# Kernel tuning notes

Measured on AMD Instinct MI355X. Metric: run time of the kernel, lower is better.

## Reference

```python
import jax, jax.numpy as jnp
import numpy as np

C_Z = 128
C_HIDDEN = 128
N_RES = 384
B = 1
EPS = 1e-5


def _layernorm(x, w, b):
    mu = jnp.mean(x, axis=-1, keepdims=True)
    var = jnp.mean(jnp.square(x - mu), axis=-1, keepdims=True)
    return (x - mu) * jax.lax.rsqrt(var + EPS) * w + b


def setup_inputs() -> dict:
    key = jax.random.key(0)
    ks = jax.random.split(key, 16)
    s_z = 1.0 / np.sqrt(C_Z)
    s_h = 1.0 / np.sqrt(C_HIDDEN)
    return {
        "z": jax.random.normal(ks[0], (B, N_RES, N_RES, C_Z), dtype=jnp.float32),
        "mask": jnp.ones((B, N_RES, N_RES), dtype=jnp.float32),
        "ln_in_w": jnp.ones((C_Z,), jnp.float32),
        "ln_in_b": jnp.zeros((C_Z,), jnp.float32),
        "a_g_w": jax.random.normal(ks[1], (C_HIDDEN, C_Z), jnp.float32) * s_z,
        "a_g_b": jnp.zeros((C_HIDDEN,), jnp.float32),
        "a_p_w": jax.random.normal(ks[2], (C_HIDDEN, C_Z), jnp.float32) * s_z,
        "a_p_b": jnp.zeros((C_HIDDEN,), jnp.float32),
        "b_g_w": jax.random.normal(ks[3], (C_HIDDEN, C_Z), jnp.float32) * s_z,
        "b_g_b": jnp.zeros((C_HIDDEN,), jnp.float32),
        "b_p_w": jax.random.normal(ks[4], (C_HIDDEN, C_Z), jnp.float32) * s_z,
        "b_p_b": jnp.zeros((C_HIDDEN,), jnp.float32),
        "g_w": jax.random.normal(ks[5], (C_Z, C_Z), jnp.float32) * s_z,
        "g_b": jnp.zeros((C_Z,), jnp.float32),
        "ln_out_w": jnp.ones((C_HIDDEN,), jnp.float32),
        "ln_out_b": jnp.zeros((C_HIDDEN,), jnp.float32),
        "z_w": jax.random.normal(ks[6], (C_Z, C_HIDDEN), jnp.float32) * s_h,
        "z_b": jnp.zeros((C_Z,), jnp.float32),
    }


def reference(z, mask, ln_in_w, ln_in_b, a_g_w, a_g_b, a_p_w, a_p_b,
              b_g_w, b_g_b, b_p_w, b_p_b, g_w, g_b,
              ln_out_w, ln_out_b, z_w, z_b):
    # z: [B, N, N, c_z]; mask: [B, N, N]
    m = mask[..., None]
    zn = _layernorm(z, ln_in_w, ln_in_b)
    # gated projections (fused LN+GEMM+sigmoid*mul in the Triton kernel)
    a = m * jax.nn.sigmoid(jnp.einsum("bijc,hc->bijh", zn, a_g_w) + a_g_b) \
          * (jnp.einsum("bijc,hc->bijh", zn, a_p_w) + a_p_b)
    b = m * jax.nn.sigmoid(jnp.einsum("bijc,hc->bijh", zn, b_g_w) + b_g_b) \
          * (jnp.einsum("bijc,hc->bijh", zn, b_p_w) + b_p_b)
    # outgoing triangle update: contract over third node k, per channel
    x = jnp.einsum("bikh,bjkh->bijh", a, b)
    # output path: sigmoid(gate(zn)) * linear_z(LN_out(x))
    xn = _layernorm(x, ln_out_w, ln_out_b)
    gate = jax.nn.sigmoid(jnp.einsum("bijc,oc->bijo", zn, g_w) + g_b)
    out = gate * (jnp.einsum("bijh,oh->bijo", xn, z_w) + z_b)
    return out
```

## Files before the change

### kernel.cpp

```cpp
#include <hip/hip_runtime.h>

#define NRES 384
#define CD   128
#define MTOT (NRES*NRES)

typedef unsigned short u16;
typedef __bf16 bf16x8 __attribute__((ext_vector_type(8)));
typedef float  f32x16 __attribute__((ext_vector_type(16)));

static __device__ __forceinline__ u16 f2bf(float f) {
  __bf16 b = (__bf16)f;
  return __builtin_bit_cast(u16, b);
}
static __device__ __forceinline__ float bf2f(u16 v) {
  return __uint_as_float(((unsigned)v) << 16);
}
static __device__ __forceinline__ float sigmoidf(float x) {
  return 1.0f / (1.0f + __expf(-x));
}

static __device__ __forceinline__ void gl16(const void* g, void* l) {
  __builtin_amdgcn_global_load_lds(
      (const __attribute__((address_space(1))) void*)g,
      (__attribute__((address_space(3))) void*)l, 16, 0, 0);
}

__global__ void k_cvt_w(const float* w0, const float* w1, const float* w2,
                        const float* w3, const float* w4, const float* w5,
                        u16* wb) {
  int i = blockIdx.x * 256 + threadIdx.x;
  const float* srcs[6] = {w0, w1, w2, w3, w4, w5};
  wb[i] = f2bf(srcs[i >> 14][i & 16383]);
}

__global__ __launch_bounds__(256) void k_ln_in(const float* __restrict__ z,
                                               const float* __restrict__ w,
                                               const float* __restrict__ b,
                                               u16* __restrict__ zn) {
  int wv = threadIdx.x >> 6, lane = threadIdx.x & 63;
  float2 wv2 = ((const float2*)w)[lane];
  float2 bv2 = ((const float2*)b)[lane];
  for (int rr = 0; rr < 4; ++rr) {
    size_t row = (size_t)blockIdx.x * 16 + wv * 4 + rr;
    float2 v = ((const float2*)(z + row * CD))[lane];
    float s = v.x + v.y;
#pragma unroll
    for (int off = 32; off >= 1; off >>= 1) s += __shfl_xor(s, off);
    float mu = s * (1.0f / CD);
    float dx = v.x - mu, dy = v.y - mu;
    float vr = dx * dx + dy * dy;
#pragma unroll
    for (int off = 32; off >= 1; off >>= 1) vr += __shfl_xor(vr, off);
    float rs = rsqrtf(vr * (1.0f / CD) + 1e-5f);
    ushort2 o;
    o.x = f2bf(dx * rs * wv2.x + bv2.x);
    o.y = f2bf(dy * rs * wv2.y + bv2.y);
    ((ushort2*)(zn + row * CD))[lane] = o;
  }
}

__global__ __launch_bounds__(256) void k_proj(
    const u16* __restrict__ zn, const float* __restrict__ mask,
    const u16* __restrict__ wb,
    const float* __restrict__ agb, const float* __restrict__ apb,
    const float* __restrict__ bgb, const float* __restrict__ bpb,
    const float* __restrict__ gb,
    u16* __restrict__ a_out, u16* __restrict__ b_out, u16* __restrict__ gate_out) {
  int type = blockIdx.y;
  int m_base = blockIdx.x * 256;
  int lane = threadIdx.x & 63;
  int wvu = __builtin_amdgcn_readfirstlane(threadIdx.x >> 6);
  int nl = lane & 31, s = lane >> 5;
  int h = wvu * 32 + nl;

  const u16 *wgp, *wpp = nullptr;
  const float *bgp, *bpp = nullptr;
  if (type == 0)      { wgp = wb;          wpp = wb + 16384; bgp = agb; bpp = apb; }
  else if (type == 1) { wgp = wb + 32768;  wpp = wb + 49152; bgp = bgb; bpp = bpb; }
  else                { wgp = wb + 65536;                    bgp = gb; }

  __shared__ u16 znt[2][64][128];

  bf16x8 wgf[8], wpf[8];
#pragma unroll
  for (int kk = 0; kk < 8; ++kk) {
    wgf[kk] = *(const bf16x8*)(wgp + h * CD + kk * 16 + s * 8);
    if (type < 2) wpf[kk] = *(const bf16x8*)(wpp + h * CD + kk * 16 + s * 8);
  }

  int rl = lane >> 4, p16 = lane & 15;
#define STAGE_ZNT(mt, bf)                                                   \
  {                                                                         \
    _Pragma("unroll")                                                       \
    for (int j = 0; j < 4; ++j) {                                           \
      int row = wvu * 16 + j * 4 + rl;                                      \
      int gc = (p16 ^ (row & 7)) << 3;                                      \
      gl16(zn + (size_t)((mt) + row) * CD + gc, &znt[bf][wvu * 16 + j * 4][0]); \
    }                                                                       \
  }

  STAGE_ZNT(m_base, 0);
  __syncthreads();

  for (int ms = 0; ms < 4; ++ms) {
    int cur = ms & 1;
    if (ms < 3) STAGE_ZNT(m_base + (ms + 1) * 64, cur ^ 1);
    int mt = m_base + ms * 64;

    if (type < 2) {
      f32x16 accg[2], accp[2];
#pragma unroll
      for (int i = 0; i < 16; ++i) { accg[0][i] = 0; accg[1][i] = 0; accp[0][i] = 0; accp[1][i] = 0; }
#pragma unroll
      for (int kk = 0; kk < 8; ++kk) {
        int c = ((kk * 2 + s) ^ (nl & 7)) << 3;
        bf16x8 zf0 = *(const bf16x8*)&znt[cur][nl][c];
        bf16x8 zf1 = *(const bf16x8*)&znt[cur][32 + nl][c];
        accg[0] = __builtin_amdgcn_mfma_f32_32x32x16_bf16(wgf[kk], zf0, accg[0], 0, 0, 0);
        accg[1] = __builtin_amdgcn_mfma_f32_32x32x16_bf16(wgf[kk], zf1, accg[1], 0, 0, 0);
        accp[0] = __builtin_amdgcn_mfma_f32_32x32x16_bf16(wpf[kk], zf0, accp[0], 0, 0, 0);
        accp[1] = __builtin_amdgcn_mfma_f32_32x32x16_bf16(wpf[kk], zf1, accp[1], 0, 0, 0);
      }
      __syncthreads();
      float mk0 = mask[mt + nl];
      float mk1 = mask[mt + 32 + nl];
      u16* outp = (type == 0) ? a_out : b_out;
#pragma unroll
      for (int r = 0; r < 16; ++r) {
        int hh = wvu * 32 + (r & 3) + 8 * (r >> 2) + 4 * s;
        float bg = bgp[hh], bp = bpp[hh];
        u16* rowp = outp + (size_t)hh * MTOT + mt + nl;
        rowp[0]  = f2bf(mk0 * sigmoidf(accg[0][r] + bg) * (accp[0][r] + bp));
        rowp[32] = f2bf(mk1 * sigmoidf(accg[1][r] + bg) * (accp[1][r] + bp));
      }
    } else {
      f32x16 accg[2];
#pragma unroll
      for (int i = 0; i < 16; ++i) { accg[0][i] = 0; accg[1][i] = 0; }
#pragma unroll
      for (int kk = 0; kk < 8; ++kk) {
        int c = ((kk * 2 + s) ^ (nl & 7)) << 3;
        bf16x8 zf0 = *(const bf16x8*)&znt[cur][nl][c];
        bf16x8 zf1 = *(const bf16x8*)&znt[cur][32 + nl][c];
        accg[0] = __builtin_amdgcn_mfma_f32_32x32x16_bf16(zf0, wgf[kk], accg[0], 0, 0, 0);
        accg[1] = __builtin_amdgcn_mfma_f32_32x32x16_bf16(zf1, wgf[kk], accg[1], 0, 0, 0);
      }
      __syncthreads();
      float bgv = bgp[h];
#pragma unroll
      for (int msb = 0; msb < 2; ++msb)
#pragma unroll
        for (int r = 0; r < 16; ++r) {
          int rowoff = (r & 3) + 8 * (r >> 2) + 4 * s;
          int mg = mt + msb * 32 + rowoff;
          gate_out[(size_t)mg * CD + h] = f2bf(sigmoidf(accg[msb][r] + bgv));
        }
    }
  }
#undef STAGE_ZNT
}

__global__ __launch_bounds__(256) void k_tri(const u16* __restrict__ a,
                                             const u16* __restrict__ b,
                                             u16* __restrict__ x) {
  int h  = blockIdx.y;
  int tm = blockIdx.x / 3, tn = blockIdx.x % 3;
  int i0 = tm * 128, j0 = tn * 128;
  const u16* ah = a + (size_t)h * MTOT;
  const u16* bh = b + (size_t)h * MTOT;

  __shared__ u16 At[128][64];
  __shared__ u16 Bt[128][64];

  int lane = threadIdx.x & 63;
  int wvu = __builtin_amdgcn_readfirstlane(threadIdx.x >> 6);
  int nl = lane & 31, s = lane >> 5;
  int wr = wvu >> 1, wc = wvu & 1;
  int rl = lane >> 3, p8 = lane & 7;

  f32x16 acc[4];
#pragma unroll
  for (int q = 0; q < 4; ++q)
#pragma unroll
    for (int i = 0; i < 16; ++i) acc[q][i] = 0;

  for (int k0 = 0; k0 < NRES; k0 += 64) {
#pragma unroll
    for (int j = 0; j < 4; ++j) {
      int row = wvu * 32 + j * 8 + rl;
      int gc = (p8 ^ (rl & 7)) << 3;
      gl16(ah + (size_t)(i0 + row) * NRES + k0 + gc, &At[wvu * 32 + j * 8][0]);
      gl16(bh + (size_t)(j0 + row) * NRES + k0 + gc, &Bt[wvu * 32 + j * 8][0]);
    }
    __syncthreads();
#pragma unroll
    for (int kk = 0; kk < 4; ++kk) {
      int c = ((kk * 2 + s) ^ (nl & 7)) << 3;
      bf16x8 af0 = *(const bf16x8*)&At[wr * 64 + nl][c];
      bf16x8 af1 = *(const bf16x8*)&At[wr * 64 + 32 + nl][c];
      bf16x8 bf0 = *(const bf16x8*)&Bt[wc * 64 + nl][c];
      bf16x8 bf1 = *(const bf16x8*)&Bt[wc * 64 + 32 + nl][c];
      acc[0] = __builtin_amdgcn_mfma_f32_32x32x16_bf16(af0, bf0, acc[0], 0, 0, 0);
      acc[1] = __builtin_amdgcn_mfma_f32_32x32x16_bf16(af0, bf1, acc[1], 0, 0, 0);
      acc[2] = __builtin_amdgcn_mfma_f32_32x32x16_bf16(af1, bf0, acc[2], 0, 0, 0);
      acc[3] = __builtin_amdgcn_mfma_f32_32x32x16_bf16(af1, bf1, acc[3], 0, 0, 0);
    }
    __syncthreads();
  }

  u16* xh = x + (size_t)h * MTOT;
#pragma unroll
  for (int msub = 0; msub < 2; ++msub)
#pragma unroll
    for (int nsub = 0; nsub < 2; ++nsub) {
      int j = j0 + wc * 64 + nsub * 32 + nl;
#pragma unroll
      for (int r = 0; r < 16; ++r) {
        int i = i0 + wr * 64 + msub * 32 + (r & 3) + 8 * (r >> 2) + 4 * s;
        xh[(size_t)i * NRES + j] = f2bf(acc[msub * 2 + nsub][r]);
      }
    }
}

__global__ __launch_bounds__(256) void k_out(
    const u16* __restrict__ x, const u16* __restrict__ gate,
    const u16* __restrict__ wb,
    const float* __restrict__ lnw, const float* __restrict__ lnb,
    const float* __restrict__ zb, float* __restrict__ out) {
  int m0 = blockIdx.x * 64;
  int t = threadIdx.x;
  int wv = t >> 6, lane = t & 63, nl = lane & 31, s = lane >> 5;
  int o = wv * 32 + nl;

  __shared__ u16 xnt[64][136];

  const u16* zwp = wb + 5 * 16384;
  bf16x8 zwf[8];
#pragma unroll
  for (int kk = 0; kk < 8; ++kk)
    zwf[kk] = *(const bf16x8*)(zwp + o * CD + kk * 16 + s * 8);

#pragma unroll
  for (int ps = 0; ps < 2; ++ps) {
    int idx = ps * 256 + t;
    int hp = idx >> 3, mc = idx & 7;
    uint4 v0 = *(const uint4*)(x + (size_t)(2 * hp)     * MTOT + m0 + mc * 8);
    uint4 v1 = *(const uint4*)(x + (size_t)(2 * hp + 1) * MTOT + m0 + mc * 8);
    unsigned c0[4] = {v0.x, v0.y, v0.z, v0.w};
    unsigned c1[4] = {v1.x, v1.y, v1.z, v1.w};
#pragma unroll
    for (int q = 0; q < 4; ++q) {
      ushort2 lo, hi;
      lo.x = (u16)(c0[q] & 0xffffu); lo.y = (u16)(c1[q] & 0xffffu);
      hi.x = (u16)(c0[q] >> 16);     hi.y = (u16)(c1[q] >> 16);
      *(ushort2*)&xnt[mc * 8 + 2 * q][2 * hp]     = lo;
      *(ushort2*)&xnt[mc * 8 + 2 * q + 1][2 * hp] = hi;
    }
  }
  __syncthreads();

  int r = t >> 2, q = t & 3;
  float vals[32];
  float sum = 0;
#pragma unroll
  for (int j = 0; j < 32; ++j) { float v = bf2f(xnt[r][q * 32 + j]); vals[j] = v; sum += v; }
  sum += __shfl_xor(sum, 1);
  sum += __shfl_xor(sum, 2);
  float mu = sum * (1.0f / CD);
  float var = 0;
#pragma unroll
  for (int j = 0; j < 32; ++j) { float d = vals[j] - mu; var += d * d; }
  var += __shfl_xor(var, 1);
  var += __shfl_xor(var, 2);
  float rs = rsqrtf(var * (1.0f / CD) + 1e-5f);
#pragma unroll
  for (int j = 0; j < 32; ++j) {
    int hh = q * 32 + j;
    xnt[r][hh] = f2bf((vals[j] - mu) * rs * lnw[hh] + lnb[hh]);
  }
  __syncthreads();

  f32x16 acc[2];
#pragma unroll
  for (int i = 0; i < 16; ++i) { acc[0][i] = 0; acc[1][i] = 0; }
#pragma unroll
  for (int kk = 0; kk < 8; ++kk) {
    bf16x8 af0 = *(const bf16x8*)&xnt[nl][kk * 16 + s * 8];
    bf16x8 af1 = *(const bf16x8*)&xnt[32 + nl][kk * 16 + s * 8];
    acc[0] = __builtin_amdgcn_mfma_f32_32x32x16_bf16(af0, zwf[kk], acc[0], 0, 0, 0);
    acc[1] = __builtin_amdgcn_mfma_f32_32x32x16_bf16(af1, zwf[kk], acc[1], 0, 0, 0);
  }

  float zbv = zb[o];
#pragma unroll
  for (int ms = 0; ms < 2; ++ms)
#pragma unroll
    for (int rr = 0; rr < 16; ++rr) {
      int rowoff = (rr & 3) + 8 * (rr >> 2) + 4 * s;
      int mg = m0 + ms * 32 + rowoff;
      float g = bf2f(gate[(size_t)mg * CD + o]);
      out[(size_t)mg * CD + o] = g * (acc[ms][rr] + zbv);
    }
}

extern "C" void kernel_launch(void* const* d_in, const int* in_sizes, int n_in,
                              void* d_out, int out_size, void* d_ws, size_t ws_size,
                              hipStream_t stream) {
  const float* z       = (const float*)d_in[0];
  const float* mask    = (const float*)d_in[1];
  const float* ln_in_w = (const float*)d_in[2];
  const float* ln_in_b = (const float*)d_in[3];
  const float* a_g_w   = (const float*)d_in[4];
  const float* a_g_b   = (const float*)d_in[5];
  const float* a_p_w   = (const float*)d_in[6];
  const float* a_p_b   = (const float*)d_in[7];
  const float* b_g_w   = (const float*)d_in[8];
  const float* b_g_b   = (const float*)d_in[9];
  const float* b_p_w   = (const float*)d_in[10];
  const float* b_p_b   = (const float*)d_in[11];
  const float* g_w     = (const float*)d_in[12];
  const float* g_b     = (const float*)d_in[13];
  const float* ln_o_w  = (const float*)d_in[14];
  const float* ln_o_b  = (const float*)d_in[15];
  const float* z_w     = (const float*)d_in[16];
  const float* z_b     = (const float*)d_in[17];
  float* out = (float*)d_out;

  const size_t SZ = (size_t)MTOT * CD * sizeof(u16);
  char* w = (char*)d_ws;
  u16* zn   = (u16*)(w);
  u16* a    = (u16*)(w + SZ);
  u16* b    = (u16*)(w + 2 * SZ);
  u16* gate = (u16*)(w + 3 * SZ);
  u16* wb   = (u16*)(w + 4 * SZ);
  (void)ws_size; (void)in_sizes; (void)n_in; (void)out_size;

  k_cvt_w<<<384, 256, 0, stream>>>(a_g_w, a_p_w, b_g_w, b_p_w, g_w, z_w, wb);
  k_ln_in<<<MTOT / 16, 256, 0, stream>>>(z, ln_in_w, ln_in_b, zn);
  k_proj<<<dim3(MTOT / 256, 3), 256, 0, stream>>>(zn, mask, wb,
      a_g_b, a_p_b, b_g_b, b_p_b, g_b, a, b, gate);
  k_tri<<<dim3(9, 128), 256, 0, stream>>>(a, b, zn);
  k_out<<<MTOT / 64, 256, 0, stream>>>(zn, gate, wb, ln_o_w, ln_o_b, z_b, out);
}
```

Before: 299.9 us.

## Fuse input LayerNorm into projection kernel and double-buffer triangle GEMM

Merges the input LayerNorm kernel into the projection kernel: each block normalizes 128 rows of z straight into padded shared memory and then computes all three projections (a, b, gate) from that tile. This removes the bf16 zn round trip through global memory and reads z only once instead of staging zn three times. The triangle kernel's K loop now double-buffers its A/B tiles so global-to-LDS loads overlap the MFMA work. In exchange, shared memory use goes up, and the projection phase loses its earlier cross-iteration prefetch and XOR swizzle, replacing the swizzle with row padding.

```diff
diff --git a/kernel.cpp b/kernel.cpp
--- a/kernel.cpp
+++ b/kernel.cpp
@@ -33,98 +33,86 @@
   wb[i] = f2bf(srcs[i >> 14][i & 16383]);
 }
 
-__global__ __launch_bounds__(256) void k_ln_in(const float* __restrict__ z,
-                                               const float* __restrict__ w,
-                                               const float* __restrict__ b,
-                                               u16* __restrict__ zn) {
-  int wv = threadIdx.x >> 6, lane = threadIdx.x & 63;
-  float2 wv2 = ((const float2*)w)[lane];
-  float2 bv2 = ((const float2*)b)[lane];
-  for (int rr = 0; rr < 4; ++rr) {
-    size_t row = (size_t)blockIdx.x * 16 + wv * 4 + rr;
-    float2 v = ((const float2*)(z + row * CD))[lane];
-    float s = v.x + v.y;
-#pragma unroll
-    for (int off = 32; off >= 1; off >>= 1) s += __shfl_xor(s, off);
-    float mu = s * (1.0f / CD);
-    float dx = v.x - mu, dy = v.y - mu;
-    float vr = dx * dx + dy * dy;
-#pragma unroll
-    for (int off = 32; off >= 1; off >>= 1) vr += __shfl_xor(vr, off);
-    float rs = rsqrtf(vr * (1.0f / CD) + 1e-5f);
-    ushort2 o;
-    o.x = f2bf(dx * rs * wv2.x + bv2.x);
-    o.y = f2bf(dy * rs * wv2.y + bv2.y);
-    ((ushort2*)(zn + row * CD))[lane] = o;
-  }
-}
-
-__global__ __launch_bounds__(256) void k_proj(
-    const u16* __restrict__ zn, const float* __restrict__ mask,
+__global__ __launch_bounds__(256) void k_fused(
+    const float* __restrict__ z, const float* __restrict__ mask,
+    const float* __restrict__ lnw, const float* __restrict__ lnb,
     const u16* __restrict__ wb,
     const float* __restrict__ agb, const float* __restrict__ apb,
     const float* __restrict__ bgb, const float* __restrict__ bpb,
     const float* __restrict__ gb,
     u16* __restrict__ a_out, u16* __restrict__ b_out, u16* __restrict__ gate_out) {
-  int type = blockIdx.y;
-  int m_base = blockIdx.x * 256;
+  int m0 = blockIdx.x * 128;
   int lane = threadIdx.x & 63;
   int wvu = __builtin_amdgcn_readfirstlane(threadIdx.x >> 6);
   int nl = lane & 31, s = lane >> 5;
   int h = wvu * 32 + nl;
 
-  const u16 *wgp, *wpp = nullptr;
-  const float *bgp, *bpp = nullptr;
-  if (type == 0)      { wgp = wb;          wpp = wb + 16384; bgp = agb; bpp = apb; }
-  else if (type == 1) { wgp = wb + 32768;  wpp = wb + 49152; bgp = bgb; bpp = bpb; }
-  else                { wgp = wb + 65536;                    bgp = gb; }
-
-  __shared__ u16 znt[2][64][128];
-
-  bf16x8 wgf[8], wpf[8];
-#pragma unroll
-  for (int kk = 0; kk < 8; ++kk) {
-    wgf[kk] = *(const bf16x8*)(wgp + h * CD + kk * 16 + s * 8);
-    if (type < 2) wpf[kk] = *(const bf16x8*)(wpp + h * CD + kk * 16 + s * 8);
-  }
-
-  int rl = lane >> 4, p16 = lane & 15;
-#define STAGE_ZNT(mt, bf)                                                   \
-  {                                                                         \
-    _Pragma("unroll")                                                       \
-    for (int j = 0; j < 4; ++j) {                                           \
-      int row = wvu * 16 + j * 4 + rl;                                      \
-      int gc = (p16 ^ (row & 7)) << 3;                                      \
-      gl16(zn + (size_t)((mt) + row) * CD + gc, &znt[bf][wvu * 16 + j * 4][0]); \
-    }                                                                       \
-  }
-
-  STAGE_ZNT(m_base, 0);
+  __shared__ u16 znt[128][136];
+
+  {
+    float4 w4 = ((const float4*)lnw)[nl];
+    float4 b4 = ((const float4*)lnb)[nl];
+#pragma unroll 4
+    for (int p = 0; p < 16; ++p) {
+      int row = wvu * 32 + p * 2 + s;
+      float4 v = ((const float4*)(z + (size_t)(m0 + row) * CD))[nl];
+      float sum = v.x + v.y + v.z + v.w;
+#pragma unroll
+      for (int off = 16; off >= 1; off >>= 1) sum += __shfl_xor(sum, off);
+      float mu = sum * (1.0f / CD);
+      float d0 = v.x - mu, d1 = v.y - mu, d2 = v.z - mu, d3 = v.w - mu;
+      float vr = d0 * d0 + d1 * d1 + d2 * d2 + d3 * d3;
+#pragma unroll
+      for (int off = 16; off >= 1; off >>= 1) vr += __shfl_xor(vr, off);
+      float rs = rsqrtf(vr * (1.0f / CD) + 1e-5f);
+      ushort4 o;
+      o.x = f2bf(d0 * rs * w4.x + b4.x);
+      o.y = f2bf(d1 * rs * w4.y + b4.y);
+      o.z = f2bf(d2 * rs * w4.z + b4.z);
+      o.w = f2bf(d3 * rs * w4.w + b4.w);
+      *(ushort4*)&znt[row][nl * 4] = o;
+    }
+  }
   __syncthreads();
 
-  for (int ms = 0; ms < 4; ++ms) {
-    int cur = ms & 1;
-    if (ms < 3) STAGE_ZNT(m_base + (ms + 1) * 64, cur ^ 1);
-    int mt = m_base + ms * 64;
-
-    if (type < 2) {
+  const u16* wgps[2] = {wb, wb + 32768};
+  const u16* wpps[2] = {wb + 16384, wb + 49152};
+  const float* bgps[2] = {agb, bgb};
+  const float* bpps[2] = {apb, bpb};
+  u16* outs[2] = {a_out, b_out};
+
+#pragma unroll
+  for (int tp = 0; tp < 2; ++tp) {
+    const u16* wgp = wgps[tp];
+    const u16* wpp = wpps[tp];
+    const float* bgp = bgps[tp];
+    const float* bpp = bpps[tp];
+    u16* outp = outs[tp];
+
+    bf16x8 wgf[8], wpf[8];
+#pragma unroll
+    for (int kk = 0; kk < 8; ++kk) {
+      wgf[kk] = *(const bf16x8*)(wgp + h * CD + kk * 16 + s * 8);
+      wpf[kk] = *(const bf16x8*)(wpp + h * CD + kk * 16 + s * 8);
+    }
+
+#pragma unroll
+    for (int msb = 0; msb < 2; ++msb) {
+      int mt = m0 + msb * 64;
       f32x16 accg[2], accp[2];
 #pragma unroll
       for (int i = 0; i < 16; ++i) { accg[0][i] = 0; accg[1][i] = 0; accp[0][i] = 0; accp[1][i] = 0; }
 #pragma unroll
       for (int kk = 0; kk < 8; ++kk) {
-        int c = ((kk * 2 + s) ^ (nl & 7)) << 3;
-        bf16x8 zf0 = *(const bf16x8*)&znt[cur][nl][c];
-        bf16x8 zf1 = *(const bf16x8*)&znt[cur][32 + nl][c];
+        bf16x8 zf0 = *(const bf16x8*)&znt[msb * 64 + nl][kk * 16 + s * 8];
+        bf16x8 zf1 = *(const bf16x8*)&znt[msb * 64 + 32 + nl][kk * 16 + s * 8];
         accg[0] = __builtin_amdgcn_mfma_f32_32x32x16_bf16(wgf[kk], zf0, accg[0], 0, 0, 0);
         accg[1] = __builtin_amdgcn_mfma_f32_32x32x16_bf16(wgf[kk], zf1, accg[1], 0, 0, 0);
         accp[0] = __builtin_amdgcn_mfma_f32_32x32x16_bf16(wpf[kk], zf0, accp[0], 0, 0, 0);
         accp[1] = __builtin_amdgcn_mfma_f32_32x32x16_bf16(wpf[kk], zf1, accp[1], 0, 0, 0);
       }
-      __syncthreads();
       float mk0 = mask[mt + nl];
       float mk1 = mask[mt + 32 + nl];
-      u16* outp = (type == 0) ? a_out : b_out;
 #pragma unroll
       for (int r = 0; r < 16; ++r) {
         int hh = wvu * 32 + (r & 3) + 8 * (r >> 2) + 4 * s;
@@ -133,31 +121,39 @@
         rowp[0]  = f2bf(mk0 * sigmoidf(accg[0][r] + bg) * (accp[0][r] + bp));
         rowp[32] = f2bf(mk1 * sigmoidf(accg[1][r] + bg) * (accp[1][r] + bp));
       }
-    } else {
+    }
+  }
+
+  {
+    const u16* wgp = wb + 65536;
+    bf16x8 wgf[8];
+#pragma unroll
+    for (int kk = 0; kk < 8; ++kk)
+      wgf[kk] = *(const bf16x8*)(wgp + h * CD + kk * 16 + s * 8);
+    float bgv = gb[h];
+#pragma unroll
+    for (int msb = 0; msb < 2; ++msb) {
+      int mt = m0 + msb * 64;
       f32x16 accg[2];
 #pragma unroll
       for (int i = 0; i < 16; ++i) { accg[0][i] = 0; accg[1][i] = 0; }
 #pragma unroll
       for (int kk = 0; kk < 8; ++kk) {
-        int c = ((kk * 2 + s) ^ (nl & 7)) << 3;
-        bf16x8 zf0 = *(const bf16x8*)&znt[cur][nl][c];
-        bf16x8 zf1 = *(const bf16x8*)&znt[cur][32 + nl][c];
+        bf16x8 zf0 = *(const bf16x8*)&znt[msb * 64 + nl][kk * 16 + s * 8];
+        bf16x8 zf1 = *(const bf16x8*)&znt[msb * 64 + 32 + nl][kk * 16 + s * 8];
         accg[0] = __builtin_amdgcn_mfma_f32_32x32x16_bf16(zf0, wgf[kk], accg[0], 0, 0, 0);
         accg[1] = __builtin_amdgcn_mfma_f32_32x32x16_bf16(zf1, wgf[kk], accg[1], 0, 0, 0);
       }
-      __syncthreads();
-      float bgv = bgp[h];
-#pragma unroll
-      for (int msb = 0; msb < 2; ++msb)
+#pragma unroll
+      for (int q = 0; q < 2; ++q)
 #pragma unroll
         for (int r = 0; r < 16; ++r) {
           int rowoff = (r & 3) + 8 * (r >> 2) + 4 * s;
-          int mg = mt + msb * 32 + rowoff;
-          gate_out[(size_t)mg * CD + h] = f2bf(sigmoidf(accg[msb][r] + bgv));
+          int mg = mt + q * 32 + rowoff;
+          gate_out[(size_t)mg * CD + h] = f2bf(sigmoidf(accg[q][r] + bgv));
         }
     }
   }
-#undef STAGE_ZNT
 }
 
 __global__ __launch_bounds__(256) void k_tri(const u16* __restrict__ a,
@@ -169,8 +165,8 @@
   const u16* ah = a + (size_t)h * MTOT;
   const u16* bh = b + (size_t)h * MTOT;
 
-  __shared__ u16 At[128][64];
-  __shared__ u16 Bt[128][64];
+  __shared__ u16 At[2][128][64];
+  __shared__ u16 Bt[2][128][64];
 
   int lane = threadIdx.x & 63;
   int wvu = __builtin_amdgcn_readfirstlane(threadIdx.x >> 6);
@@ -184,22 +180,30 @@
 #pragma unroll
     for (int i = 0; i < 16; ++i) acc[q][i] = 0;
 
-  for (int k0 = 0; k0 < NRES; k0 += 64) {
-#pragma unroll
-    for (int j = 0; j < 4; ++j) {
-      int row = wvu * 32 + j * 8 + rl;
-      int gc = (p8 ^ (rl & 7)) << 3;
-      gl16(ah + (size_t)(i0 + row) * NRES + k0 + gc, &At[wvu * 32 + j * 8][0]);
-      gl16(bh + (size_t)(j0 + row) * NRES + k0 + gc, &Bt[wvu * 32 + j * 8][0]);
-    }
-    __syncthreads();
+#define STAGE_TRI(bf, k0)                                                     \
+  {                                                                           \
+    _Pragma("unroll")                                                         \
+    for (int j = 0; j < 4; ++j) {                                             \
+      int row = wvu * 32 + j * 8 + rl;                                        \
+      int gc = (p8 ^ (rl & 7)) << 3;                                          \
+      gl16(ah + (size_t)(i0 + row) * NRES + (k0) + gc, &At[bf][wvu * 32 + j * 8][0]); \
+      gl16(bh + (size_t)(j0 + row) * NRES + (k0) + gc, &Bt[bf][wvu * 32 + j * 8][0]); \
+    }                                                                         \
+  }
+
+  STAGE_TRI(0, 0);
+  __syncthreads();
+
+  for (int kb = 0; kb < 6; ++kb) {
+    int cur = kb & 1;
+    if (kb < 5) STAGE_TRI(cur ^ 1, (kb + 1) * 64);
 #pragma unroll
     for (int kk = 0; kk < 4; ++kk) {
       int c = ((kk * 2 + s) ^ (nl & 7)) << 3;
-      bf16x8 af0 = *(const bf16x8*)&At[wr * 64 + nl][c];
-      bf16x8 af1 = *(const bf16x8*)&At[wr * 64 + 32 + nl][c];
-      bf16x8 bf0 = *(const bf16x8*)&Bt[wc * 64 + nl][c];
-      bf16x8 bf1 = *(const bf16x8*)&Bt[wc * 64 + 32 + nl][c];
+      bf16x8 af0 = *(const bf16x8*)&At[cur][wr * 64 + nl][c];
+      bf16x8 af1 = *(const bf16x8*)&At[cur][wr * 64 + 32 + nl][c];
+      bf16x8 bf0 = *(const bf16x8*)&Bt[cur][wc * 64 + nl][c];
+      bf16x8 bf1 = *(const bf16x8*)&Bt[cur][wc * 64 + 32 + nl][c];
       acc[0] = __builtin_amdgcn_mfma_f32_32x32x16_bf16(af0, bf0, acc[0], 0, 0, 0);
       acc[1] = __builtin_amdgcn_mfma_f32_32x32x16_bf16(af0, bf1, acc[1], 0, 0, 0);
       acc[2] = __builtin_amdgcn_mfma_f32_32x32x16_bf16(af1, bf0, acc[2], 0, 0, 0);
@@ -207,6 +211,7 @@
     }
     __syncthreads();
   }
+#undef STAGE_TRI
 
   u16* xh = x + (size_t)h * MTOT;
 #pragma unroll
@@ -328,7 +333,7 @@
 
   const size_t SZ = (size_t)MTOT * CD * sizeof(u16);
   char* w = (char*)d_ws;
-  u16* zn   = (u16*)(w);
+  u16* x    = (u16*)(w);
   u16* a    = (u16*)(w + SZ);
   u16* b    = (u16*)(w + 2 * SZ);
   u16* gate = (u16*)(w + 3 * SZ);
@@ -336,9 +341,8 @@
   (void)ws_size; (void)in_sizes; (void)n_in; (void)out_size;
 
   k_cvt_w<<<384, 256, 0, stream>>>(a_g_w, a_p_w, b_g_w, b_p_w, g_w, z_w, wb);
-  k_ln_in<<<MTOT / 16, 256, 0, stream>>>(z, ln_in_w, ln_in_b, zn);
-  k_proj<<<dim3(MTOT / 256, 3), 256, 0, stream>>>(zn, mask, wb,
+  k_fused<<<MTOT / 128, 256, 0, stream>>>(z, mask, ln_in_w, ln_in_b, wb,
       a_g_b, a_p_b, b_g_b, b_p_b, g_b, a, b, gate);
-  k_tri<<<dim3(9, 128), 256, 0, stream>>>(a, b, zn);
-  k_out<<<MTOT / 64, 256, 0, stream>>>(zn, gate, wb, ln_o_w, ln_o_b, z_b, out);
-}
+  k_tri<<<dim3(9, 128), 256, 0, stream>>>(a, b, x);
+  k_out<<<MTOT / 64, 256, 0, stream>>>(x, gate, wb, ln_o_w, ln_o_b, z_b, out);
+}
```

After: 323.7 us. 1.08x slower.

## Fuse gate projection into output kernel and double-buffer triangle GEMM

Applied to the files above, without the earlier changes.

The gate projection and its sigmoid move out of k_proj into k_out, which reloads zn, computes the gate with MFMA and applies it directly. This removes the bf16 gate tensor write and read round trip, and x now gets its own workspace buffer instead of overwriting zn. The triangle kernel also gets double-buffered LDS staging, so loads of the next k-chunk overlap the MFMAs on the current one. The cost is extra zn reads and more registers in k_out, and twice the LDS in k_tri, which may lower occupancy.

```diff
diff --git a/kernel.cpp b/kernel.cpp
--- a/kernel.cpp
+++ b/kernel.cpp
@@ -64,8 +64,7 @@
     const u16* __restrict__ wb,
     const float* __restrict__ agb, const float* __restrict__ apb,
     const float* __restrict__ bgb, const float* __restrict__ bpb,
-    const float* __restrict__ gb,
-    u16* __restrict__ a_out, u16* __restrict__ b_out, u16* __restrict__ gate_out) {
+    u16* __restrict__ a_out, u16* __restrict__ b_out) {
   int type = blockIdx.y;
   int m_base = blockIdx.x * 256;
   int lane = threadIdx.x & 63;
@@ -73,11 +72,11 @@
   int nl = lane & 31, s = lane >> 5;
   int h = wvu * 32 + nl;
 
-  const u16 *wgp, *wpp = nullptr;
-  const float *bgp, *bpp = nullptr;
-  if (type == 0)      { wgp = wb;          wpp = wb + 16384; bgp = agb; bpp = apb; }
-  else if (type == 1) { wgp = wb + 32768;  wpp = wb + 49152; bgp = bgb; bpp = bpb; }
-  else                { wgp = wb + 65536;                    bgp = gb; }
+  const u16* wgp = (type == 0) ? wb : wb + 32768;
+  const u16* wpp = (type == 0) ? wb + 16384 : wb + 49152;
+  const float* bgp = (type == 0) ? agb : bgb;
+  const float* bpp = (type == 0) ? apb : bpb;
+  u16* outp = (type == 0) ? a_out : b_out;
 
   __shared__ u16 znt[2][64][128];
 
@@ -85,7 +84,7 @@
 #pragma unroll
   for (int kk = 0; kk < 8; ++kk) {
     wgf[kk] = *(const bf16x8*)(wgp + h * CD + kk * 16 + s * 8);
-    if (type < 2) wpf[kk] = *(const bf16x8*)(wpp + h * CD + kk * 16 + s * 8);
+    wpf[kk] = *(const bf16x8*)(wpp + h * CD + kk * 16 + s * 8);
   }
 
   int rl = lane >> 4, p16 = lane & 15;
@@ -107,54 +106,29 @@
     if (ms < 3) STAGE_ZNT(m_base + (ms + 1) * 64, cur ^ 1);
     int mt = m_base + ms * 64;
 
-    if (type < 2) {
-      f32x16 accg[2], accp[2];
-#pragma unroll
-      for (int i = 0; i < 16; ++i) { accg[0][i] = 0; accg[1][i] = 0; accp[0][i] = 0; accp[1][i] = 0; }
-#pragma unroll
-      for (int kk = 0; kk < 8; ++kk) {
-        int c = ((kk * 2 + s) ^ (nl & 7)) << 3;
-        bf16x8 zf0 = *(const bf16x8*)&znt[cur][nl][c];
-        bf16x8 zf1 = *(const bf16x8*)&znt[cur][32 + nl][c];
-        accg[0] = __builtin_amdgcn_mfma_f32_32x32x16_bf16(wgf[kk], zf0, accg[0], 0, 0, 0);
-        accg[1] = __builtin_amdgcn_mfma_f32_32x32x16_bf16(wgf[kk], zf1, accg[1], 0, 0, 0);
-        accp[0] = __builtin_amdgcn_mfma_f32_32x32x16_bf16(wpf[kk], zf0, accp[0], 0, 0, 0);
-        accp[1] = __builtin_amdgcn_mfma_f32_32x32x16_bf16(wpf[kk], zf1, accp[1], 0, 0, 0);
-      }
-      __syncthreads();
-      float mk0 = mask[mt + nl];
-      float mk1 = mask[mt + 32 + nl];
-      u16* outp = (type == 0) ? a_out : b_out;
-#pragma unroll
-      for (int r = 0; r < 16; ++r) {
-        int hh = wvu * 32 + (r & 3) + 8 * (r >> 2) + 4 * s;
-        float bg = bgp[hh], bp = bpp[hh];
-        u16* rowp = outp + (size_t)hh * MTOT + mt + nl;
-        rowp[0]  = f2bf(mk0 * sigmoidf(accg[0][r] + bg) * (accp[0][r] + bp));
-        rowp[32] = f2bf(mk1 * sigmoidf(accg[1][r] + bg) * (accp[1][r] + bp));
-      }
-    } else {
-      f32x16 accg[2];
-#pragma unroll
-      for (int i = 0; i < 16; ++i) { accg[0][i] = 0; accg[1][i] = 0; }
-#pragma unroll
-      for (int kk = 0; kk < 8; ++kk) {
-        int c = ((kk * 2 + s) ^ (nl & 7)) << 3;
-        bf16x8 zf0 = *(const bf16x8*)&znt[cur][nl][c];
-        bf16x8 zf1 = *(const bf16x8*)&znt[cur][32 + nl][c];
-        accg[0] = __builtin_amdgcn_mfma_f32_32x32x16_bf16(zf0, wgf[kk], accg[0], 0, 0, 0);
-        accg[1] = __builtin_amdgcn_mfma_f32_32x32x16_bf16(zf1, wgf[kk], accg[1], 0, 0, 0);
-      }
-      __syncthreads();
-      float bgv = bgp[h];
-#pragma unroll
-      for (int msb = 0; msb < 2; ++msb)
-#pragma unroll
-        for (int r = 0; r < 16; ++r) {
-          int rowoff = (r & 3) + 8 * (r >> 2) + 4 * s;
-          int mg = mt + msb * 32 + rowoff;
-          gate_out[(size_t)mg * CD + h] = f2bf(sigmoidf(accg[msb][r] + bgv));
-        }
+    f32x16 accg[2], accp[2];
+#pragma unroll
+    for (int i = 0; i < 16; ++i) { accg[0][i] = 0; accg[1][i] = 0; accp[0][i] = 0; accp[1][i] = 0; }
+#pragma unroll
+    for (int kk = 0; kk < 8; ++kk) {
+      int c = ((kk * 2 + s) ^ (nl & 7)) << 3;
+      bf16x8 zf0 = *(const bf16x8*)&znt[cur][nl][c];
+      bf16x8 zf1 = *(const bf16x8*)&znt[cur][32 + nl][c];
+      accg[0] = __builtin_amdgcn_mfma_f32_32x32x16_bf16(wgf[kk], zf0, accg[0], 0, 0, 0);
+      accg[1] = __builtin_amdgcn_mfma_f32_32x32x16_bf16(wgf[kk], zf1, accg[1], 0, 0, 0);
+      accp[0] = __builtin_amdgcn_mfma_f32_32x32x16_bf16(wpf[kk], zf0, accp[0], 0, 0, 0);
+      accp[1] = __builtin_amdgcn_mfma_f32_32x32x16_bf16(wpf[kk], zf1, accp[1], 0, 0, 0);
+    }
+    __syncthreads();
+    float mk0 = mask[mt + nl];
+    float mk1 = mask[mt + 32 + nl];
+#pragma unroll
+    for (int r = 0; r < 16; ++r) {
+      int hh = wvu * 32 + (r & 3) + 8 * (r >> 2) + 4 * s;
+      float bg = bgp[hh], bp = bpp[hh];
+      u16* rowp = outp + (size_t)hh * MTOT + mt + nl;
+      rowp[0]  = f2bf(mk0 * sigmoidf(accg[0][r] + bg) * (accp[0][r] + bp));
+      rowp[32] = f2bf(mk1 * sigmoidf(accg[1][r] + bg) * (accp[1][r] + bp));
     }
   }
 #undef STAGE_ZNT
@@ -169,8 +143,8 @@
   const u16* ah = a + (size_t)h * MTOT;
   const u16* bh = b + (size_t)h * MTOT;
 
-  __shared__ u16 At[128][64];
-  __shared__ u16 Bt[128][64];
+  __shared__ u16 At[2][128][64];
+  __shared__ u16 Bt[2][128][64];
 
   int lane = threadIdx.x & 63;
   int wvu = __builtin_amdgcn_readfirstlane(threadIdx.x >> 6);
@@ -184,22 +158,30 @@
 #pragma unroll
     for (int i = 0; i < 16; ++i) acc[q][i] = 0;
 
-  for (int k0 = 0; k0 < NRES; k0 += 64) {
-#pragma unroll
-    for (int j = 0; j < 4; ++j) {
-      int row = wvu * 32 + j * 8 + rl;
-      int gc = (p8 ^ (rl & 7)) << 3;
-      gl16(ah + (size_t)(i0 + row) * NRES + k0 + gc, &At[wvu * 32 + j * 8][0]);
-      gl16(bh + (size_t)(j0 + row) * NRES + k0 + gc, &Bt[wvu * 32 + j * 8][0]);
-    }
-    __syncthreads();
+#define STAGE_TRI(bf, k0)                                                     \
+  {                                                                           \
+    _Pragma("unroll")                                                         \
+    for (int j = 0; j < 4; ++j) {                                             \
+      int row = wvu * 32 + j * 8 + rl;                                        \
+      int gc = (p8 ^ (rl & 7)) << 3;                                          \
+      gl16(ah + (size_t)(i0 + row) * NRES + (k0) + gc, &At[bf][wvu * 32 + j * 8][0]); \
+      gl16(bh + (size_t)(j0 + row) * NRES + (k0) + gc, &Bt[bf][wvu * 32 + j * 8][0]); \
+    }                                                                         \
+  }
+
+  STAGE_TRI(0, 0);
+  __syncthreads();
+
+  for (int kb = 0; kb < 6; ++kb) {
+    int cur = kb & 1;
+    if (kb < 5) STAGE_TRI(cur ^ 1, (kb + 1) * 64);
 #pragma unroll
     for (int kk = 0; kk < 4; ++kk) {
       int c = ((kk * 2 + s) ^ (nl & 7)) << 3;
-      bf16x8 af0 = *(const bf16x8*)&At[wr * 64 + nl][c];
-      bf16x8 af1 = *(const bf16x8*)&At[wr * 64 + 32 + nl][c];
-      bf16x8 bf0 = *(const bf16x8*)&Bt[wc * 64 + nl][c];
-      bf16x8 bf1 = *(const bf16x8*)&Bt[wc * 64 + 32 + nl][c];
+      bf16x8 af0 = *(const bf16x8*)&At[cur][wr * 64 + nl][c];
+      bf16x8 af1 = *(const bf16x8*)&At[cur][wr * 64 + 32 + nl][c];
+      bf16x8 bf0 = *(const bf16x8*)&Bt[cur][wc * 64 + nl][c];
+      bf16x8 bf1 = *(const bf16x8*)&Bt[cur][wc * 64 + 32 + nl][c];
       acc[0] = __builtin_amdgcn_mfma_f32_32x32x16_bf16(af0, bf0, acc[0], 0, 0, 0);
       acc[1] = __builtin_amdgcn_mfma_f32_32x32x16_bf16(af0, bf1, acc[1], 0, 0, 0);
       acc[2] = __builtin_amdgcn_mfma_f32_32x32x16_bf16(af1, bf0, acc[2], 0, 0, 0);
@@ -207,6 +189,7 @@
     }
     __syncthreads();
   }
+#undef STAGE_TRI
 
   u16* xh = x + (size_t)h * MTOT;
 #pragma unroll
@@ -223,8 +206,8 @@
 }
 
 __global__ __launch_bounds__(256) void k_out(
-    const u16* __restrict__ x, const u16* __restrict__ gate,
-    const u16* __restrict__ wb,
+    const u16* __restrict__ x, const u16* __restrict__ zn,
+    const u16* __restrict__ wb, const float* __restrict__ gb,
     const float* __restrict__ lnw, const float* __restrict__ lnb,
     const float* __restrict__ zb, float* __restrict__ out) {
   int m0 = blockIdx.x * 64;
@@ -232,9 +215,44 @@
   int wv = t >> 6, lane = t & 63, nl = lane & 31, s = lane >> 5;
   int o = wv * 32 + nl;
 
-  __shared__ u16 xnt[64][136];
-
+  __shared__ u16 tile[64][136];
+
+  const u16* gwp = wb + 4 * 16384;
   const u16* zwp = wb + 5 * 16384;
+
+  bf16x8 gwf[8];
+#pragma unroll
+  for (int kk = 0; kk < 8; ++kk)
+    gwf[kk] = *(const bf16x8*)(gwp + o * CD + kk * 16 + s * 8);
+
+#pragma unroll
+  for (int it = 0; it < 4; ++it) {
+    int idx = it * 256 + t;
+    int r = idx >> 4, c8 = idx & 15;
+    *(uint4*)&tile[r][c8 * 8] =
+        *(const uint4*)(zn + (size_t)(m0 + r) * CD + c8 * 8);
+  }
+  __syncthreads();
+
+  f32x16 gacc[2];
+#pragma unroll
+  for (int i = 0; i < 16; ++i) { gacc[0][i] = 0; gacc[1][i] = 0; }
+#pragma unroll
+  for (int kk = 0; kk < 8; ++kk) {
+    bf16x8 zf0 = *(const bf16x8*)&tile[nl][kk * 16 + s * 8];
+    bf16x8 zf1 = *(const bf16x8*)&tile[32 + nl][kk * 16 + s * 8];
+    gacc[0] = __builtin_amdgcn_mfma_f32_32x32x16_bf16(zf0, gwf[kk], gacc[0], 0, 0, 0);
+    gacc[1] = __builtin_amdgcn_mfma_f32_32x32x16_bf16(zf1, gwf[kk], gacc[1], 0, 0, 0);
+  }
+  float gbv = gb[o];
+  float gv[32];
+#pragma unroll
+  for (int ms = 0; ms < 2; ++ms)
+#pragma unroll
+    for (int r = 0; r < 16; ++r)
+      gv[ms * 16 + r] = sigmoidf(gacc[ms][r] + gbv);
+  __syncthreads();
+
   bf16x8 zwf[8];
 #pragma unroll
   for (int kk = 0; kk < 8; ++kk)
@@ -253,8 +271,8 @@
       ushort2 lo, hi;
       lo.x = (u16)(c0[q] & 0xffffu); lo.y = (u16)(c1[q] & 0xffffu);
       hi.x = (u16)(c0[q] >> 16);     hi.y = (u16)(c1[q] >> 16);
-      *(ushort2*)&xnt[mc * 8 + 2 * q][2 * hp]     = lo;
-      *(ushort2*)&xnt[mc * 8 + 2 * q + 1][2 * hp] = hi;
+      *(ushort2*)&tile[mc * 8 + 2 * q][2 * hp]     = lo;
+      *(ushort2*)&tile[mc * 8 + 2 * q + 1][2 * hp] = hi;
     }
   }
   __syncthreads();
@@ -263,7 +281,7 @@
   float vals[32];
   float sum = 0;
 #pragma unroll
-  for (int j = 0; j < 32; ++j) { float v = bf2f(xnt[r][q * 32 + j]); vals[j] = v; sum += v; }
+  for (int j = 0; j < 32; ++j) { float v = bf2f(tile[r][q * 32 + j]); vals[j] = v; sum += v; }
   sum += __shfl_xor(sum, 1);
   sum += __shfl_xor(sum, 2);
   float mu = sum * (1.0f / CD);
@@ -276,7 +294,7 @@
 #pragma unroll
   for (int j = 0; j < 32; ++j) {
     int hh = q * 32 + j;
-    xnt[r][hh] = f2bf((vals[j] - mu) * rs * lnw[hh] + lnb[hh]);
+    tile[r][hh] = f2bf((vals[j] - mu) * rs * lnw[hh] + lnb[hh]);
   }
   __syncthreads();
 
@@ -285,8 +303,8 @@
   for (int i = 0; i < 16; ++i) { acc[0][i] = 0; acc[1][i] = 0; }
 #pragma unroll
   for (int kk = 0; kk < 8; ++kk) {
-    bf16x8 af0 = *(const bf16x8*)&xnt[nl][kk * 16 + s * 8];
-    bf16x8 af1 = *(const bf16x8*)&xnt[32 + nl][kk * 16 + s * 8];
+    bf16x8 af0 = *(const bf16x8*)&tile[nl][kk * 16 + s * 8];
+    bf16x8 af1 = *(const bf16x8*)&tile[32 + nl][kk * 16 + s * 8];
     acc[0] = __builtin_amdgcn_mfma_f32_32x32x16_bf16(af0, zwf[kk], acc[0], 0, 0, 0);
     acc[1] = __builtin_amdgcn_mfma_f32_32x32x16_bf16(af1, zwf[kk], acc[1], 0, 0, 0);
   }
@@ -298,8 +316,7 @@
     for (int rr = 0; rr < 16; ++rr) {
       int rowoff = (rr & 3) + 8 * (rr >> 2) + 4 * s;
       int mg = m0 + ms * 32 + rowoff;
-      float g = bf2f(gate[(size_t)mg * CD + o]);
-      out[(size_t)mg * CD + o] = g * (acc[ms][rr] + zbv);
+      out[(size_t)mg * CD + o] = gv[ms * 16 + rr] * (acc[ms][rr] + zbv);
     }
 }
 
@@ -328,17 +345,17 @@
 
   const size_t SZ = (size_t)MTOT * CD * sizeof(u16);
   char* w = (char*)d_ws;
-  u16* zn   = (u16*)(w);
-  u16* a    = (u16*)(w + SZ);
-  u16* b    = (u16*)(w + 2 * SZ);
-  u16* gate = (u16*)(w + 3 * SZ);
-  u16* wb   = (u16*)(w + 4 * SZ);
+  u16* zn = (u16*)(w);
+  u16* a  = (u16*)(w + SZ);
+  u16* b  = (u16*)(w + 2 * SZ);
+  u16* x  = (u16*)(w + 3 * SZ);
+  u16* wb = (u16*)(w + 4 * SZ);
   (void)ws_size; (void)in_sizes; (void)n_in; (void)out_size;
 
   k_cvt_w<<<384, 256, 0, stream>>>(a_g_w, a_p_w, b_g_w, b_p_w, g_w, z_w, wb);
   k_ln_in<<<MTOT / 16, 256, 0, stream>>>(z, ln_in_w, ln_in_b, zn);
-  k_proj<<<dim3(MTOT / 256, 3), 256, 0, stream>>>(zn, mask, wb,
-      a_g_b, a_p_b, b_g_b, b_p_b, g_b, a, b, gate);
-  k_tri<<<dim3(9, 128), 256, 0, stream>>>(a, b, zn);
-  k_out<<<MTOT / 64, 256, 0, stream>>>(zn, gate, wb, ln_o_w, ln_o_b, z_b, out);
-}
+  k_proj<<<dim3(MTOT / 256, 2), 256, 0, stream>>>(zn, mask, wb,
+      a_g_b, a_p_b, b_g_b, b_p_b, a, b);
+  k_tri<<<dim3(9, 128), 256, 0, stream>>>(a, b, x);
+  k_out<<<MTOT / 64, 256, 0, stream>>>(x, zn, wb, g_b, ln_o_w, ln_o_b, z_b, out);
+}
```

Result: no change. 297.8 us (-0.7%).
